# Kernel optimization log

Measured on AMD Instinct MI355X. Metric: run time of the kernel, lower is better.

The kernel has to match this reference:

```python
import jax, jax.numpy as jnp
import numpy as np

N_NODES = 50000
N_EDGES = 1600000
IN_FEATS = 256
OUT_FEATS = 64


def setup_inputs() -> dict:
    key = jax.random.key(0)
    k_x, k_w, k_b, k_s, k_d = jax.random.split(key, 5)
    x = jax.random.normal(k_x, (N_NODES, IN_FEATS), dtype=jnp.float32)
    # nn.Linear(in_feats, out_feats): weight [out, in], bias [out]
    W = jax.random.normal(k_w, (OUT_FEATS, IN_FEATS), dtype=jnp.float32) / np.sqrt(IN_FEATS)
    b = jax.random.normal(k_b, (OUT_FEATS,), dtype=jnp.float32) * 0.01
    edge_src = jax.random.randint(k_s, (N_EDGES,), 0, N_NODES, dtype=jnp.int32)
    edge_dst = jax.random.randint(k_d, (N_EDGES,), 0, N_NODES, dtype=jnp.int32)
    return {"x": x, "W": W, "b": b, "edge_src": edge_src, "edge_dst": edge_dst}


def reference(x, W, b, edge_src, edge_dst):
    # h = dropout(relu(Linear(x)))  -- dropout p=0 (eval) => identity
    h = jax.nn.relu(x @ W.T + b)                     # [N, out_feats]
    # update_all: message = h[src], reduce = mean over incoming edges per dst
    msg = h[edge_src]                                # [E, out_feats] gather
    summed = jax.ops.segment_sum(msg, edge_dst, num_segments=N_NODES)  # [N, out]
    deg = jax.ops.segment_sum(jnp.ones((edge_src.shape[0],), dtype=h.dtype),
                              edge_dst, num_segments=N_NODES)          # [N]
    deg = jnp.maximum(deg, 1.0)
    return summed / deg[:, None]
```

## Files before the change

### kernel.cpp

```cpp
#include <hip/hip_runtime.h>
#include <hip/hip_bf16.h>

#define K_IN 256
#define O_OUT 64
#define NBINS 1024
#define NPB 49
#define CAP 1824
#define PART_CHUNK 4096
#define WS_STRIDE 264
#define XS_STRIDE 136

typedef __attribute__((ext_vector_type(8))) short short8;
typedef __attribute__((ext_vector_type(4))) float f32x4;

__device__ inline unsigned short bf16bits(float a) {
  __hip_bfloat16 t = __float2bfloat16(a);
  return *(unsigned short*)&t;
}

__global__ __launch_bounds__(256) void k_prep(const float* __restrict__ W,
                                              unsigned short* __restrict__ Wb,
                                              int* __restrict__ cursor) {
  int i = blockIdx.x * 256 + threadIdx.x;
  Wb[i] = bf16bits(W[i]);
  if (i < NBINS) cursor[i] = 0;
}

struct GemmSmem {
  unsigned short wsb[64 * WS_STRIDE];
  unsigned short xs[64 * XS_STRIDE];
};
struct PartSmem {
  int cnt[NBINS];
  int scanb[NBINS];
  int gbase[NBINS];
  int wsum[4];
  unsigned ord[PART_CHUNK];
  unsigned short obin[PART_CHUNK];
};
union FusedSmem {
  GemmSmem g;
  PartSmem p;
};

__device__ void gemm_body(GemmSmem& sm, int gid, const float* __restrict__ x,
                          const unsigned short* __restrict__ Wb,
                          const float* __restrict__ bias,
                          __hip_bfloat16* __restrict__ h, int N) {
  const int tid = threadIdx.x;
  const int lane = tid & 63;
  const int wv = tid >> 6;
  const int n0 = gid * 64;

  {
    const unsigned* wsrc = (const unsigned*)Wb;
    unsigned* wdst = (unsigned*)sm.wsb;
#pragma unroll
    for (int r = 0; r < 32; ++r) {
      int flat = r * 256 + tid;
      int row = flat >> 7;
      int col = flat & 127;
      wdst[row * (WS_STRIDE / 2) + col] = wsrc[flat];
    }
  }

  f32x4 acc[4] = {{0.f, 0.f, 0.f, 0.f}, {0.f, 0.f, 0.f, 0.f},
                  {0.f, 0.f, 0.f, 0.f}, {0.f, 0.f, 0.f, 0.f}};

  for (int kc = 0; kc < K_IN; kc += 128) {
    __syncthreads();
    unsigned* xdst = (unsigned*)sm.xs;
#pragma unroll
    for (int r = 0; r < 8; ++r) {
      int flat = r * 256 + tid;
      int row = flat >> 5;
      int c4 = flat & 31;
      float4 v = make_float4(0.f, 0.f, 0.f, 0.f);
      int node = n0 + row;
      if (node < N) v = *(const float4*)(x + (size_t)node * K_IN + kc + c4 * 4);
      unsigned u0 = (unsigned)bf16bits(v.x) | ((unsigned)bf16bits(v.y) << 16);
      unsigned u1 = (unsigned)bf16bits(v.z) | ((unsigned)bf16bits(v.w) << 16);
      xdst[row * (XS_STRIDE / 2) + c4 * 2] = u0;
      xdst[row * (XS_STRIDE / 2) + c4 * 2 + 1] = u1;
    }
    __syncthreads();

    const unsigned short* arow =
        sm.xs + (wv * 16 + (lane & 15)) * XS_STRIDE + (lane >> 4) * 8;
    const unsigned short* bcol =
        sm.wsb + (lane & 15) * WS_STRIDE + kc + (lane >> 4) * 8;
#pragma unroll
    for (int k0 = 0; k0 < 128; k0 += 32) {
      short8 a = *(const short8*)(arow + k0);
#pragma unroll
      for (int nt = 0; nt < 4; ++nt) {
        short8 bfr = *(const short8*)(bcol + nt * 16 * WS_STRIDE + k0);
        acc[nt] = __builtin_amdgcn_mfma_f32_16x16x32_bf16(a, bfr, acc[nt], 0, 0, 0);
      }
    }
  }

  const int col = lane & 15;
  const int rbase = (lane >> 4) * 4;
#pragma unroll
  for (int nt = 0; nt < 4; ++nt) {
    float bv = bias[nt * 16 + col];
#pragma unroll
    for (int j = 0; j < 4; ++j) {
      int node = n0 + wv * 16 + rbase + j;
      if (node < N) {
        float v = fmaxf(acc[nt][j] + bv, 0.f);
        h[(size_t)node * O_OUT + nt * 16 + col] = __float2bfloat16(v);
      }
    }
  }
}

__device__ void part_body(PartSmem& sm, int pid, const int* __restrict__ esrc,
                          const int* __restrict__ edst, int* __restrict__ cursor,
                          unsigned* __restrict__ bucket, int E) {
  const int tid = threadIdx.x;
  const int lane = tid & 63;
  const int wid = tid >> 6;
  const int base = pid * PART_CHUNK;

#pragma unroll
  for (int r = 0; r < 4; ++r) sm.cnt[r * 256 + tid] = 0;
  __syncthreads();

  unsigned pk[16];
  int bn[16];
  int rk[16];
#pragma unroll
  for (int r = 0; r < 4; ++r) {
    int e0 = base + r * 1024 + tid * 4;
    int4 s4, d4;
    if (e0 + 3 < E) {
      s4 = *(const int4*)(esrc + e0);
      d4 = *(const int4*)(edst + e0);
    } else {
      s4 = make_int4(0, 0, 0, 0);
      d4 = make_int4(0, 0, 0, 0);
      int* sp = (int*)&s4;
      int* dp = (int*)&d4;
      for (int j = 0; j < 4; ++j)
        if (e0 + j < E) { sp[j] = esrc[e0 + j]; dp[j] = edst[e0 + j]; }
    }
    const int* sp = (const int*)&s4;
    const int* dp = (const int*)&d4;
#pragma unroll
    for (int j = 0; j < 4; ++j) {
      int k = r * 4 + j;
      int e = e0 + j;
      if (e < E) {
        int s = sp[j];
        int d = dp[j];
        int bb = (int)__umulhi((unsigned)d, 87652394u);
        int dl = d - bb * NPB;
        pk[k] = (unsigned)s | ((unsigned)dl << 16);
        bn[k] = bb;
        rk[k] = atomicAdd(&sm.cnt[bb], 1);
      } else {
        bn[k] = -1;
      }
    }
  }
  __syncthreads();

  int c0 = sm.cnt[4 * tid];
  int c1 = sm.cnt[4 * tid + 1];
  int c2 = sm.cnt[4 * tid + 2];
  int c3 = sm.cnt[4 * tid + 3];
  int s = c0 + c1 + c2 + c3;
  int incl = s;
#pragma unroll
  for (int off = 1; off < 64; off <<= 1) {
    int t = __shfl_up(incl, off);
    if (lane >= off) incl += t;
  }
  if (lane == 63) sm.wsum[wid] = incl;
  __syncthreads();
  int wpre = 0;
  for (int w = 0; w < wid; ++w) wpre += sm.wsum[w];
  int excl = wpre + incl - s;
  sm.scanb[4 * tid] = excl;
  sm.scanb[4 * tid + 1] = excl + c0;
  sm.scanb[4 * tid + 2] = excl + c0 + c1;
  sm.scanb[4 * tid + 3] = excl + c0 + c1 + c2;
  sm.gbase[4 * tid] = (c0 > 0) ? atomicAdd(&cursor[4 * tid], c0) : 0;
  sm.gbase[4 * tid + 1] = (c1 > 0) ? atomicAdd(&cursor[4 * tid + 1], c1) : 0;
  sm.gbase[4 * tid + 2] = (c2 > 0) ? atomicAdd(&cursor[4 * tid + 2], c2) : 0;
  sm.gbase[4 * tid + 3] = (c3 > 0) ? atomicAdd(&cursor[4 * tid + 3], c3) : 0;
  __syncthreads();

#pragma unroll
  for (int k = 0; k < 16; ++k) {
    if (bn[k] >= 0) {
      int pos = sm.scanb[bn[k]] + rk[k];
      sm.ord[pos] = pk[k];
      sm.obin[pos] = (unsigned short)bn[k];
    }
  }
  __syncthreads();

  int nv = E - base;
  if (nv > PART_CHUNK) nv = PART_CHUNK;
  for (int p = tid; p < nv; p += 256) {
    int bb = sm.obin[p];
    int slot = sm.gbase[bb] + (p - sm.scanb[bb]);
    if (slot < CAP) bucket[(size_t)bb * CAP + slot] = sm.ord[p];
  }
}

__global__ __launch_bounds__(256) void k_fused(const float* __restrict__ x,
                                               const unsigned short* __restrict__ Wb,
                                               const float* __restrict__ bias,
                                               __hip_bfloat16* __restrict__ h,
                                               const int* __restrict__ esrc,
                                               const int* __restrict__ edst,
                                               int* __restrict__ cursor,
                                               unsigned* __restrict__ bucket,
                                               int N, int E) {
  __shared__ FusedSmem sm;
  const int npart = (E + PART_CHUNK - 1) / PART_CHUNK;
  const int b = blockIdx.x;
  if (b % 3 == 1 && b / 3 < npart) {
    part_body(sm.p, b / 3, esrc, edst, cursor, bucket, E);
  } else {
    int skipped = (b + 2) / 3;
    if (skipped > npart) skipped = npart;
    gemm_body(sm.g, b - skipped, x, Wb, bias, h, N);
  }
}

__global__ __launch_bounds__(512) void k_sortagg(const unsigned* __restrict__ bucket,
                                                 const int* __restrict__ cursor,
                                                 const unsigned* __restrict__ h32,
                                                 float* __restrict__ out, int N) {
  __shared__ int hist[NPB];
  __shared__ int offs[NPB];
  __shared__ unsigned short sbuf[CAP];

  const int tid = threadIdx.x;
  const int lane = tid & 63;
  const int wid = tid >> 6;
  const int bin = blockIdx.x;

  if (tid < NPB) hist[tid] = 0;
  __syncthreads();

  int cnt = cursor[bin];
  if (cnt > CAP) cnt = CAP;
  const unsigned* bb = bucket + (size_t)bin * CAP;

  unsigned pk[4];
  int rk[4];
  {
    int i0 = tid * 4;
    uint4 v;
    if (i0 + 3 < cnt) {
      v = *(const uint4*)(bb + i0);
    } else {
      v = make_uint4(0, 0, 0, 0);
      unsigned* vp = (unsigned*)&v;
      for (int j = 0; j < 4; ++j)
        if (i0 + j < cnt) vp[j] = bb[i0 + j];
    }
    const unsigned* vp = (const unsigned*)&v;
#pragma unroll
    for (int j = 0; j < 4; ++j) {
      if (i0 + j < cnt) {
        pk[j] = vp[j];
        rk[j] = atomicAdd(&hist[vp[j] >> 16], 1);
      } else {
        rk[j] = -1;
      }
    }
  }
  __syncthreads();

  if (tid < 64) {
    int hval = (tid < NPB) ? hist[tid] : 0;
    int incl = hval;
#pragma unroll
    for (int off = 1; off < 64; off <<= 1) {
      int t = __shfl_up(incl, off);
      if (lane >= off) incl += t;
    }
    if (tid < NPB) offs[tid] = incl - hval;
  }
  __syncthreads();

#pragma unroll
  for (int j = 0; j < 4; ++j) {
    if (rk[j] >= 0) sbuf[offs[pk[j] >> 16] + rk[j]] = (unsigned short)(pk[j] & 0xFFFFu);
  }
  __syncthreads();

  const int half = lane >> 5;
  const int hl = lane & 31;
  for (int nl = wid; nl < NPB; nl += 8) {
    int n = bin * NPB + nl;
    if (n >= N) break;
    int c = hist[nl];
    const unsigned short* bs = sbuf + offs[nl];

    float ax = 0.f, ay = 0.f;
    const int npairs = c >> 1;
    const int g8 = npairs & ~7;
    if (g8 > 0) {
      int p[8];
#pragma unroll
      for (int k = 0; k < 8; ++k) p[k] = bs[2 * k + half];
      for (int i = 8;; i += 8) {
        int q[8];
        bool more = (i < g8);
        if (more) {
#pragma unroll
          for (int k = 0; k < 8; ++k) q[k] = bs[2 * (i + k) + half];
        }
#pragma unroll
        for (int k = 0; k < 8; ++k) {
          unsigned u = h32[(size_t)p[k] * 32 + hl];
          ax += __uint_as_float(u << 16);
          ay += __uint_as_float(u & 0xFFFF0000u);
        }
        if (!more) break;
#pragma unroll
        for (int k = 0; k < 8; ++k) p[k] = q[k];
      }
    }
    for (int j = g8; j < npairs; ++j) {
      int p = bs[2 * j + half];
      unsigned u = h32[(size_t)p * 32 + hl];
      ax += __uint_as_float(u << 16);
      ay += __uint_as_float(u & 0xFFFF0000u);
    }
    if (c & 1) {
      int p = bs[c - 1];
      if (half == 0) {
        unsigned u = h32[(size_t)p * 32 + hl];
        ax += __uint_as_float(u << 16);
        ay += __uint_as_float(u & 0xFFFF0000u);
      }
    }

    float bx = __shfl(ax, lane ^ 32);
    float by = __shfl(ay, lane ^ 32);
    if (half == 0) {
      float inv = 1.f / fmaxf((float)c, 1.f);
      float2 r;
      r.x = (ax + bx) * inv;
      r.y = (ay + by) * inv;
      ((float2*)out)[(size_t)n * 32 + hl] = r;
    }
  }
}

extern "C" void kernel_launch(void* const* d_in, const int* in_sizes, int n_in,
                              void* d_out, int out_size, void* d_ws, size_t ws_size,
                              hipStream_t stream) {
  const float* x = (const float*)d_in[0];
  const float* W = (const float*)d_in[1];
  const float* b = (const float*)d_in[2];
  const int* esrc = (const int*)d_in[3];
  const int* edst = (const int*)d_in[4];
  float* out = (float*)d_out;

  const int N = in_sizes[0] / K_IN;
  const int E = in_sizes[3];

  char* ws = (char*)d_ws;
  unsigned short* Wb = (unsigned short*)ws;
  __hip_bfloat16* h = (__hip_bfloat16*)(ws + 32768);
  size_t off = 32768 + (size_t)N * O_OUT * sizeof(__hip_bfloat16);
  int* cursor = (int*)(ws + off);
  off += NBINS * sizeof(int);
  unsigned* bucket = (unsigned*)(ws + off);

  const int ngemm = (N + 63) / 64;
  const int npart = (E + PART_CHUNK - 1) / PART_CHUNK;

  k_prep<<<(K_IN * O_OUT) / 256, 256, 0, stream>>>(W, Wb, cursor);
  k_fused<<<ngemm + npart, 256, 0, stream>>>(x, Wb, b, h, esrc, edst, cursor,
                                             bucket, N, E);
  k_sortagg<<<NBINS, 512, 0, stream>>>(bucket, cursor, (const unsigned*)h, out, N);
}
```

Before: 168.0 us.

## Cut fused-kernel LDS, read W from global, widen aggregation gathers to 8 bytes

```diff
diff --git a/kernel.cpp b/kernel.cpp
--- a/kernel.cpp
+++ b/kernel.cpp
@@ -7,7 +7,6 @@
 #define NPB 49
 #define CAP 1824
 #define PART_CHUNK 4096
-#define WS_STRIDE 264
 #define XS_STRIDE 136
 
 typedef __attribute__((ext_vector_type(8))) short short8;
@@ -27,7 +26,6 @@
 }
 
 struct GemmSmem {
-  unsigned short wsb[64 * WS_STRIDE];
   unsigned short xs[64 * XS_STRIDE];
 };
 struct PartSmem {
@@ -36,7 +34,6 @@
   int gbase[NBINS];
   int wsum[4];
   unsigned ord[PART_CHUNK];
-  unsigned short obin[PART_CHUNK];
 };
 union FusedSmem {
   GemmSmem g;
@@ -52,20 +49,9 @@
   const int wv = tid >> 6;
   const int n0 = gid * 64;
 
-  {
-    const unsigned* wsrc = (const unsigned*)Wb;
-    unsigned* wdst = (unsigned*)sm.wsb;
-#pragma unroll
-    for (int r = 0; r < 32; ++r) {
-      int flat = r * 256 + tid;
-      int row = flat >> 7;
-      int col = flat & 127;
-      wdst[row * (WS_STRIDE / 2) + col] = wsrc[flat];
-    }
-  }
-
   f32x4 acc[4] = {{0.f, 0.f, 0.f, 0.f}, {0.f, 0.f, 0.f, 0.f},
                   {0.f, 0.f, 0.f, 0.f}, {0.f, 0.f, 0.f, 0.f}};
+  const unsigned short* wbase = Wb + (lane & 15) * K_IN + (lane >> 4) * 8;
 
   for (int kc = 0; kc < K_IN; kc += 128) {
     __syncthreads();
@@ -87,14 +73,12 @@
 
     const unsigned short* arow =
         sm.xs + (wv * 16 + (lane & 15)) * XS_STRIDE + (lane >> 4) * 8;
-    const unsigned short* bcol =
-        sm.wsb + (lane & 15) * WS_STRIDE + kc + (lane >> 4) * 8;
 #pragma unroll
     for (int k0 = 0; k0 < 128; k0 += 32) {
       short8 a = *(const short8*)(arow + k0);
 #pragma unroll
       for (int nt = 0; nt < 4; ++nt) {
-        short8 bfr = *(const short8*)(bcol + nt * 16 * WS_STRIDE + k0);
+        short8 bfr = *(const short8*)(wbase + nt * 16 * K_IN + kc + k0);
         acc[nt] = __builtin_amdgcn_mfma_f32_16x16x32_bf16(a, bfr, acc[nt], 0, 0, 0);
       }
     }
@@ -157,7 +141,7 @@
         int d = dp[j];
         int bb = (int)__umulhi((unsigned)d, 87652394u);
         int dl = d - bb * NPB;
-        pk[k] = (unsigned)s | ((unsigned)dl << 16);
+        pk[k] = (unsigned)s | ((unsigned)dl << 16) | ((unsigned)bb << 22);
         bn[k] = bb;
         rk[k] = atomicAdd(&sm.cnt[bb], 1);
       } else {
@@ -198,7 +182,6 @@
     if (bn[k] >= 0) {
       int pos = sm.scanb[bn[k]] + rk[k];
       sm.ord[pos] = pk[k];
-      sm.obin[pos] = (unsigned short)bn[k];
     }
   }
   __syncthreads();
@@ -206,21 +189,22 @@
   int nv = E - base;
   if (nv > PART_CHUNK) nv = PART_CHUNK;
   for (int p = tid; p < nv; p += 256) {
-    int bb = sm.obin[p];
+    unsigned v = sm.ord[p];
+    int bb = v >> 22;
     int slot = sm.gbase[bb] + (p - sm.scanb[bb]);
-    if (slot < CAP) bucket[(size_t)bb * CAP + slot] = sm.ord[p];
-  }
-}
-
-__global__ __launch_bounds__(256) void k_fused(const float* __restrict__ x,
-                                               const unsigned short* __restrict__ Wb,
-                                               const float* __restrict__ bias,
-                                               __hip_bfloat16* __restrict__ h,
-                                               const int* __restrict__ esrc,
-                                               const int* __restrict__ edst,
-                                               int* __restrict__ cursor,
-                                               unsigned* __restrict__ bucket,
-                                               int N, int E) {
+    if (slot < CAP) bucket[(size_t)bb * CAP + slot] = v;
+  }
+}
+
+__global__ __launch_bounds__(256, 5) void k_fused(const float* __restrict__ x,
+                                                  const unsigned short* __restrict__ Wb,
+                                                  const float* __restrict__ bias,
+                                                  __hip_bfloat16* __restrict__ h,
+                                                  const int* __restrict__ esrc,
+                                                  const int* __restrict__ edst,
+                                                  int* __restrict__ cursor,
+                                                  unsigned* __restrict__ bucket,
+                                                  int N, int E) {
   __shared__ FusedSmem sm;
   const int npart = (E + PART_CHUNK - 1) / PART_CHUNK;
   const int b = blockIdx.x;
@@ -239,7 +223,7 @@
                                                  float* __restrict__ out, int N) {
   __shared__ int hist[NPB];
   __shared__ int offs[NPB];
-  __shared__ unsigned short sbuf[CAP];
+  __shared__ unsigned short sbuf[CAP + 64];
 
   const int tid = threadIdx.x;
   const int lane = tid & 63;
@@ -271,7 +255,7 @@
     for (int j = 0; j < 4; ++j) {
       if (i0 + j < cnt) {
         pk[j] = vp[j];
-        rk[j] = atomicAdd(&hist[vp[j] >> 16], 1);
+        rk[j] = atomicAdd(&hist[(vp[j] >> 16) & 63], 1);
       } else {
         rk[j] = -1;
       }
@@ -293,66 +277,51 @@
 
 #pragma unroll
   for (int j = 0; j < 4; ++j) {
-    if (rk[j] >= 0) sbuf[offs[pk[j] >> 16] + rk[j]] = (unsigned short)(pk[j] & 0xFFFFu);
-  }
-  __syncthreads();
-
-  const int half = lane >> 5;
-  const int hl = lane & 31;
+    if (rk[j] >= 0)
+      sbuf[offs[(pk[j] >> 16) & 63] + rk[j]] = (unsigned short)(pk[j] & 0xFFFFu);
+  }
+  __syncthreads();
+
+  const int q = lane >> 4;
+  const int hl = lane & 15;
+  const uint2* __restrict__ h2 = (const uint2*)h32;
+
   for (int nl = wid; nl < NPB; nl += 8) {
     int n = bin * NPB + nl;
     if (n >= N) break;
     int c = hist[nl];
     const unsigned short* bs = sbuf + offs[nl];
 
-    float ax = 0.f, ay = 0.f;
-    const int npairs = c >> 1;
-    const int g8 = npairs & ~7;
-    if (g8 > 0) {
+    float a0 = 0.f, a1 = 0.f, a2 = 0.f, a3 = 0.f;
+    const int nqc = (c + 3) >> 2;
+    for (int i0 = 0; i0 < nqc; i0 += 8) {
       int p[8];
 #pragma unroll
-      for (int k = 0; k < 8; ++k) p[k] = bs[2 * k + half];
-      for (int i = 8;; i += 8) {
-        int q[8];
-        bool more = (i < g8);
-        if (more) {
-#pragma unroll
-          for (int k = 0; k < 8; ++k) q[k] = bs[2 * (i + k) + half];
-        }
-#pragma unroll
-        for (int k = 0; k < 8; ++k) {
-          unsigned u = h32[(size_t)p[k] * 32 + hl];
-          ax += __uint_as_float(u << 16);
-          ay += __uint_as_float(u & 0xFFFF0000u);
-        }
-        if (!more) break;
-#pragma unroll
-        for (int k = 0; k < 8; ++k) p[k] = q[k];
-      }
-    }
-    for (int j = g8; j < npairs; ++j) {
-      int p = bs[2 * j + half];
-      unsigned u = h32[(size_t)p * 32 + hl];
-      ax += __uint_as_float(u << 16);
-      ay += __uint_as_float(u & 0xFFFF0000u);
-    }
-    if (c & 1) {
-      int p = bs[c - 1];
-      if (half == 0) {
-        unsigned u = h32[(size_t)p * 32 + hl];
-        ax += __uint_as_float(u << 16);
-        ay += __uint_as_float(u & 0xFFFF0000u);
-      }
-    }
-
-    float bx = __shfl(ax, lane ^ 32);
-    float by = __shfl(ay, lane ^ 32);
-    if (half == 0) {
+      for (int k = 0; k < 8; ++k) {
+        int e = (i0 + k) * 4 + q;
+        p[k] = (e < c) ? (int)bs[e] : 0;
+      }
+#pragma unroll
+      for (int k = 0; k < 8; ++k) {
+        float wk = ((i0 + k) * 4 + q < c) ? 1.f : 0.f;
+        uint2 u = h2[p[k] * 16 + hl];
+        a0 = fmaf(wk, __uint_as_float(u.x << 16), a0);
+        a1 = fmaf(wk, __uint_as_float(u.x & 0xFFFF0000u), a1);
+        a2 = fmaf(wk, __uint_as_float(u.y << 16), a2);
+        a3 = fmaf(wk, __uint_as_float(u.y & 0xFFFF0000u), a3);
+      }
+    }
+
+    a0 += __shfl_xor(a0, 16); a1 += __shfl_xor(a1, 16);
+    a2 += __shfl_xor(a2, 16); a3 += __shfl_xor(a3, 16);
+    a0 += __shfl_xor(a0, 32); a1 += __shfl_xor(a1, 32);
+    a2 += __shfl_xor(a2, 32); a3 += __shfl_xor(a3, 32);
+
+    if (lane < 16) {
       float inv = 1.f / fmaxf((float)c, 1.f);
-      float2 r;
-      r.x = (ax + bx) * inv;
-      r.y = (ay + by) * inv;
-      ((float2*)out)[(size_t)n * 32 + hl] = r;
+      float4 r;
+      r.x = a0 * inv; r.y = a1 * inv; r.z = a2 * inv; r.w = a3 * inv;
+      *(float4*)(out + (size_t)n * O_OUT + hl * 4) = r;
     }
   }
 }
```

Result: slower. 174.8 us (+4.0%).
